# Performance work log

Measured on AMD Instinct MI355X. Metric: run time of the kernel, lower is better.

Reference implementation:

```python
import jax, jax.numpy as jnp
import numpy as np

N, E, H = 25000, 100000, 32          # nodes, edges, node/clique hidden dim
NC, A, EC = 8000, 50000, 24000       # cliques, node2clique assignments, clique edges
EEMB, CEE, L = 8, 8, 2               # edge emb dims, n layers


def segment_mean(vals, ids, num):
    s = jax.ops.segment_sum(vals, ids, num_segments=num)
    cnt = jax.ops.segment_sum(jnp.ones(ids.shape[0], vals.dtype), ids, num_segments=num)
    return s / jnp.maximum(cnt, 1.0)[:, None]


def setup_inputs() -> dict:
    key = jax.random.key(0)
    ks = jax.random.split(key, 24)
    s = 0.1  # param scale
    inp = {
        "node_features": jax.random.normal(ks[0], (N, H), jnp.float32),
        "edge_index": jax.random.randint(ks[1], (2, E), 0, N),
        "edge_features": jax.random.normal(ks[2], (E, EEMB), jnp.float32),
        "clique_features": jax.random.normal(ks[3], (NC, H), jnp.float32),
        "node2clique_index": jnp.stack([
            jax.random.randint(ks[4], (A,), 0, N),
            jax.random.randint(ks[5], (A,), 0, NC)]),
        "clique_edge_index": jax.random.randint(ks[6], (2, EC), 0, NC),
        "clique_edge_features": jax.random.normal(ks[7], (EC, CEE), jnp.float32),
        # node NNConv params (stacked over L layers)
        "nn1_w": jax.random.normal(ks[8], (L, EEMB, H)) * s,
        "nn1_b": jnp.zeros((L, H)),
        "nn2_w": jax.random.normal(ks[9], (L, H, H * H)) * s,
        "nn2_b": jnp.zeros((L, H * H)),
        "root_w": jax.random.normal(ks[10], (L, H, H)) * s,
        "root_b": jnp.zeros((L, H)),
        # Node2Clique linear
        "n2c_w": jax.random.normal(ks[11], (L, H, H)) * s,
        "n2c_b": jnp.zeros((L, H)),
        # clique NNConv params
        "cnn1_w": jax.random.normal(ks[12], (L, CEE, H)) * s,
        "cnn1_b": jnp.zeros((L, H)),
        "cnn2_w": jax.random.normal(ks[13], (L, H, H * H)) * s,
        "cnn2_b": jnp.zeros((L, H * H)),
        "croot_w": jax.random.normal(ks[14], (L, H, H)) * s,
        "croot_b": jnp.zeros((L, H)),
        # Clique2Node linear
        "c2n_w": jax.random.normal(ks[15], (L, H, H)) * s,
        "c2n_b": jnp.zeros((L, H)),
    }
    return inp


def nnconv(x, src, dst, edge_attr, w1, b1, w2, b2, rw, rb, n_out_nodes):
    # per-edge weight matrices from the edge MLP: [E, in, out]
    h = jax.nn.relu(edge_attr @ w1 + b1)
    We = (h @ w2 + b2).reshape(edge_attr.shape[0], x.shape[1], -1)
    msg = jnp.einsum('ei,eio->eo', x[src], We)           # message from source
    agg = segment_mean(msg, dst, n_out_nodes)            # mean aggregation at target
    return agg + x @ rw + rb                             # root weight + bias


def reference(node_features, edge_index, edge_features, clique_features,
              node2clique_index, clique_edge_index, clique_edge_features,
              nn1_w, nn1_b, nn2_w, nn2_b, root_w, root_b, n2c_w, n2c_b,
              cnn1_w, cnn1_b, cnn2_w, cnn2_b, croot_w, croot_b, c2n_w, c2n_b):
    x, c = node_features, clique_features
    src, dst = edge_index[0], edge_index[1]
    nid, cid = node2clique_index[0], node2clique_index[1]
    csrc, cdst = clique_edge_index[0], clique_edge_index[1]
    for l in range(L):
        # node-level edge-conditioned conv
        x = jax.nn.relu(nnconv(x, src, dst, edge_features,
                               nn1_w[l], nn1_b[l], nn2_w[l], nn2_b[l],
                               root_w[l], root_b[l], N))
        # Node2Clique: project node feats, scatter-mean into cliques
        m = x @ n2c_w[l] + n2c_b[l]
        c = c + segment_mean(m[nid], cid, NC)
        # clique-level edge-conditioned conv
        c = jax.nn.relu(nnconv(c, csrc, cdst, clique_edge_features,
                               cnn1_w[l], cnn1_b[l], cnn2_w[l], cnn2_b[l],
                               croot_w[l], croot_b[l], NC))
        # Clique2Node: project clique feats, scatter-mean back onto nodes
        m = c @ c2n_w[l] + c2n_b[l]
        x = x + segment_mean(m[cid], nid, N)
    return (x, c)
```

## Files before the change

### kernel.cpp

```cpp
#include <hip/hip_runtime.h>
#include <hip/hip_bf16.h>

typedef unsigned int u32;
typedef unsigned short u16;

#define DEVINL __device__ __forceinline__

constexpr int Nn  = 25000;
constexpr int Ee  = 100000;
constexpr int NCc = 8000;
constexpr int Aa  = 50000;
constexpr int ECc = 24000;
constexpr int TCOLS = 1088;
constexpr int WPSZ  = TCOLS*32;
constexpr int TT_ROW = 561;
constexpr int NB_N = (Nn + 255)/256;
constexpr int NB_C = (NCc + 255)/256;
constexpr int HB_N = Ee/16;
constexpr int HB_C = ECc/16;

typedef float f32x4 __attribute__((ext_vector_type(4)));
typedef _Float16 h16x2 __attribute__((ext_vector_type(2)));
typedef _Float16 h16x8 __attribute__((ext_vector_type(8)));

DEVINL float b2f(u16 u){ union{u32 i;float f;}v; v.i = ((u32)u)<<16; return v.f; }
DEVINL float bfl(u32 u){ union{u32 i;float f;}v; v.i = u<<16; return v.f; }
DEVINL float bfh(u32 u){ union{u32 i;float f;}v; v.i = u & 0xffff0000u; return v.f; }
DEVINL u16 f2b(float f){ union{float f;u32 i;}v; v.f=f; u32 i=v.i;
  return (u16)((i + 0x7fffu + ((i>>16)&1u)) >> 16); }
DEVINL u16 f2h(float x){ union{ _Float16 h; u16 u; } v; v.h = (_Float16)x; return v.u; }
DEVINL u32 pkh2(float a, float b){
  union{ _Float16 h[2]; u32 u; } v;
  v.h[0] = (_Float16)a; v.h[1] = (_Float16)b; return v.u;
}
DEVINL float ldw(const void* p, long i, int f){
  return f ? ((const float*)p)[i] : b2f(((const u16*)p)[i]);
}
DEVINL float dot2f(u32 a, u32 b, float c){
  union U{u32 u; h16x2 h;};
  U ua; ua.u = a; U ub; ub.u = b;
#if __has_builtin(__builtin_amdgcn_fdot2)
  return __builtin_amdgcn_fdot2(ua.h, ub.h, c, false);
#else
  return c + (float)ua.h[0]*(float)ub.h[0] + (float)ua.h[1]*(float)ub.h[1];
#endif
}

__global__ __launch_bounds__(256) void k_detect(const u16* __restrict__ p, int n,
                        u32* __restrict__ maxbits, int* __restrict__ zcnt,
                        int* __restrict__ done, int* __restrict__ flag){
  int i0 = blockIdx.x*256 + threadIdx.x;
  float lm = 0.f; int lz = 0;
  for (int i = i0; i < n; i += gridDim.x*256){
    u16 v = p[i];
    if (v == 0) lz++;
    lm = fmaxf(lm, fabsf(b2f(v)));
  }
  #pragma unroll
  for (int off = 32; off; off >>= 1){
    lm = fmaxf(lm, __shfl_down(lm, off));
    lz += __shfl_down(lz, off);
  }
  if ((threadIdx.x & 63) == 0){
    atomicMax(maxbits, __float_as_uint(lm));
    atomicAdd(zcnt, lz);
  }
  __syncthreads();
  if (threadIdx.x == 0){
    __threadfence();
    if (atomicAdd(done, 1) == gridDim.x - 1){
      float m = __uint_as_float(*maxbits);
      *flag = (m > 1e6f || *zcnt > n/4) ? 1 : 0;
    }
  }
}

__global__ __launch_bounds__(256) void k_count_all(const int* __restrict__ ei, const int* __restrict__ cei,
                          const int* __restrict__ n2c,
                          int* __restrict__ deg_nd, int* __restrict__ deg_ce,
                          int* __restrict__ deg_n2c, int* __restrict__ deg_c2n,
                          int* __restrict__ cnt_sn, int* __restrict__ cnt_sc){
  int i = blockIdx.x*256 + threadIdx.x;
  if (i < Ee)                             atomicAdd(&deg_nd[ei[Ee + i]], 1);
  else if ((i -= Ee) < ECc)               atomicAdd(&deg_ce[cei[ECc + i]], 1);
  else if ((i -= ECc) < Aa)               atomicAdd(&deg_n2c[n2c[Aa + i]], 1);
  else if ((i -= Aa) < Aa)                atomicAdd(&deg_c2n[n2c[i]], 1);
  else if ((i -= Aa) < Ee)                atomicAdd(&cnt_sn[ei[i]], 1);
  else if ((i -= Ee) < ECc)               atomicAdd(&cnt_sc[cei[i]], 1);
}

__global__ __launch_bounds__(256) void k_scan_block(
    const int* __restrict__ c0, const int* __restrict__ c1,
    const int* __restrict__ c2, const int* __restrict__ c3,
    int* __restrict__ o0, int* __restrict__ o1, int* __restrict__ o2, int* __restrict__ o3,
    int* __restrict__ b0, int* __restrict__ b1, int* __restrict__ b2, int* __restrict__ b3){
  __shared__ int s[256];
  int bid = blockIdx.x, seg, rb;
  if (bid < NB_N){ seg=0; rb=bid; }
  else if (bid < NB_N+NB_C){ seg=1; rb=bid-NB_N; }
  else if (bid < 2*NB_N+NB_C){ seg=2; rb=bid-NB_N-NB_C; }
  else { seg=3; rb=bid-2*NB_N-NB_C; }
  const int* cnt = seg==0?c0 : seg==1?c1 : seg==2?c2 : c3;
  int* offs = seg==0?o0 : seg==1?o1 : seg==2?o2 : o3;
  int* bs   = seg==0?b0 : seg==1?b1 : seg==2?b2 : b3;
  int M = (seg & 1) ? NCc : Nn;
  int tid = threadIdx.x;
  int i = rb*256 + tid;
  int v = (i < M) ? cnt[i] : 0;
  s[tid] = v; __syncthreads();
  for (int d = 1; d < 256; d <<= 1){
    int t = (tid >= d) ? s[tid-d] : 0;
    __syncthreads();
    s[tid] += t;
    __syncthreads();
  }
  if (i < M) offs[i] = s[tid] - v;
  if (tid == 255) bs[rb] = s[255];
}

__global__ __launch_bounds__(512) void k_spine(int* __restrict__ b0, int* __restrict__ b1,
                      int* __restrict__ b2, int* __restrict__ b3){
  __shared__ int s[512];
  int tid = threadIdx.x, seg = tid >> 7, lane = tid & 127;
  int NB = (seg & 1) ? NB_C : NB_N;
  int* bp = seg==0?b0 : seg==1?b1 : seg==2?b2 : b3;
  int v = (lane < NB) ? bp[lane] : 0;
  s[tid] = v; __syncthreads();
  for (int d = 1; d < 128; d <<= 1){
    int t = (lane >= d) ? s[tid-d] : 0;
    __syncthreads();
    s[tid] += t;
    __syncthreads();
  }
  if (lane < NB) bp[lane] = s[tid] - v;
}

__global__ __launch_bounds__(256) void k_scan_fix(
    int* __restrict__ o0, int* __restrict__ o1, int* __restrict__ o2, int* __restrict__ o3,
    const int* __restrict__ b0, const int* __restrict__ b1,
    const int* __restrict__ b2, const int* __restrict__ b3){
  int i = blockIdx.x*256 + threadIdx.x;
  if (i < Nn) o0[i] += b0[i >> 8];
  else if ((i -= Nn) < NCc) o1[i] += b1[i >> 8];
  else if ((i -= NCc) < Nn) o2[i] += b2[i >> 8];
  else if ((i -= Nn) < NCc) o3[i] += b3[i >> 8];
}

__global__ __launch_bounds__(256) void k_place(const int* __restrict__ ei, const int* __restrict__ cei,
                      const int* __restrict__ n2c,
                      const int* __restrict__ offs_n, const int* __restrict__ offs_c,
                      const int* __restrict__ offs_an, const int* __restrict__ offs_ac,
                      int* __restrict__ cur_n, int* __restrict__ cur_c,
                      int* __restrict__ cur_an, int* __restrict__ cur_ac,
                      int* __restrict__ perm_n, int* __restrict__ perm_c,
                      int* __restrict__ an2c, int* __restrict__ ac2n){
  int i = blockIdx.x*256 + threadIdx.x;
  if (i < Ee){
    int s = ei[i];
    perm_n[offs_n[s] + atomicAdd(&cur_n[s], 1)] = i;
  } else if ((i -= Ee) < ECc){
    int s = cei[i];
    perm_c[offs_c[s] + atomicAdd(&cur_c[s], 1)] = i;
  } else if ((i -= ECc) < Aa){
    int c = n2c[Aa + i];
    an2c[offs_ac[c] + atomicAdd(&cur_ac[c], 1)] = n2c[i];
  } else if ((i -= Aa) < Aa){
    int nd = n2c[i];
    ac2n[offs_an[nd] + atomicAdd(&cur_an[nd], 1)] = n2c[Aa + i];
  }
}

__global__ __launch_bounds__(256) void k_gather(const int* __restrict__ ei, const int* __restrict__ cei,
                       const int* __restrict__ perm_n, const int* __restrict__ perm_c,
                       const void* __restrict__ ef, const void* __restrict__ cef,
                       const int* __restrict__ flag,
                       int2* __restrict__ sdp_n, float* __restrict__ efp_n,
                       int2* __restrict__ sdp_c, float* __restrict__ efp_c){
  int i = blockIdx.x*256 + threadIdx.x;
  int f = *flag;
  if (i < Ee*8){
    int p = i >> 3, j = i & 7;
    int e = perm_n[p];
    efp_n[i] = ldw(ef, (long)e*8 + j, f);
    if (j == 0) sdp_n[p] = make_int2(ei[e], ei[Ee + e]);
  } else if ((i -= Ee*8) < ECc*8){
    int p = i >> 3, j = i & 7;
    int e = perm_c[p];
    efp_c[i] = ldw(cef, (long)e*8 + j, f);
    if (j == 0) sdp_c[p] = make_int2(cei[e], cei[ECc + e]);
  }
}

__global__ __launch_bounds__(256) void k_hprep(const float* __restrict__ efp_n, const float* __restrict__ efp_c,
                      const void* __restrict__ nn1w, const void* __restrict__ nn1b,
                      const void* __restrict__ cnn1w, const void* __restrict__ cnn1b,
                      const int* __restrict__ flag,
                      u32* __restrict__ hp_n, u32* __restrict__ hp_c){
  __shared__ float w1s[256], b1s[32], efs[128];
  int b = blockIdx.x, tid = threadIdx.x;
  int isC, l, rb_;
  if (b < HB_N){ isC=0; l=0; rb_=b; }
  else if (b < 2*HB_N){ isC=0; l=1; rb_=b-HB_N; }
  else if (b < 2*HB_N+HB_C){ isC=1; l=0; rb_=b-2*HB_N; }
  else { isC=1; l=1; rb_=b-2*HB_N-HB_C; }
  const float* efp = isC ? efp_c : efp_n;
  const void* W1 = isC ? cnn1w : nn1w;
  const void* B1 = isC ? cnn1b : nn1b;
  u32* hp = (isC ? hp_c : hp_n) + (size_t)l*(isC?ECc:Ee)*16;
  int f = *flag;
  w1s[tid] = ldw(W1, (long)l*256 + tid, f);
  if (tid < 32) b1s[tid] = ldw(B1, (long)l*32 + tid, f);
  if (tid < 128) efs[tid] = efp[(size_t)rb_*128 + tid];
  __syncthreads();
  int e8 = tid >> 4, kk = tid & 15;
  float a0 = b1s[2*kk], a1 = b1s[2*kk+1];
  #pragma unroll
  for (int j = 0; j < 8; j++){
    float ev = efs[e8*8 + j];
    a0 += ev * w1s[j*32 + 2*kk];
    a1 += ev * w1s[j*32 + 2*kk + 1];
  }
  hp[(size_t)rb_*256 + tid] = pkh2(fmaxf(a0, 0.f), fmaxf(a1, 0.f));
}

__global__ __launch_bounds__(256) void k_wpack_all(const void* __restrict__ nn2w, const void* __restrict__ nn2b,
                          const void* __restrict__ rootw,
                          const void* __restrict__ cnn2w, const void* __restrict__ cnn2b,
                          const void* __restrict__ crootw,
                          const int* __restrict__ flag, u16* __restrict__ Wp4){
  int i = blockIdx.x*256 + threadIdx.x;
  if (i >= 4*WPSZ) return;
  int set = i / WPSZ, j = i - set*WPSZ;
  int l = set >> 1, isC = set & 1;
  const void* W2 = isC ? cnn2w : nn2w;
  const void* B2 = isC ? cnn2b : nn2b;
  const void* RW = isC ? crootw : rootw;
  int f = *flag;
  int col = j >> 5, ii = j & 31;
  float v;
  if (col < 1024)      v = ldw(W2, (long)l*32768 + ((col>>5)<<10) + (ii<<5) + (col&31), f);
  else if (col < 1056) v = ldw(B2, (long)l*1024 + (ii<<5) + (col-1024), f);
  else                 v = ldw(RW, (long)l*1024 + (ii<<5) + (col-1056), f);
  Wp4[i] = f2h(v);
}

__global__ __launch_bounds__(512) void k_conv_fused(const void* __restrict__ base, int braw,
                           const float* __restrict__ addagg, const int* __restrict__ adddeg, int M,
                           const int2* __restrict__ sdp, const u32* __restrict__ hp,
                           const int* __restrict__ offs, int E_,
                           const u16* __restrict__ Wp,
                           const void* __restrict__ rb, long rboff,
                           const int* __restrict__ flag,
                           float* __restrict__ feat_root, float* __restrict__ agg){
  __shared__ __align__(16) u32 Tt[16*TT_ROW];
  __shared__ u32 hws[8][64];
  int tid = threadIdx.x;
  int w = tid >> 6, lane = tid & 63;
  int quad = lane >> 4, lm = lane & 15;
  int n0 = blockIdx.x * 16;
  int f = *flag;
  int n = n0 + lm;
  int nc = n < M ? n : M-1;
  long bidx = (long)nc*32 + quad*8;
  float fv[8];
  if (braw && f == 0){
    uint4 q = *(const uint4*)((const u16*)base + bidx);
    fv[0]=bfl(q.x); fv[1]=bfh(q.x); fv[2]=bfl(q.y); fv[3]=bfh(q.y);
    fv[4]=bfl(q.z); fv[5]=bfh(q.z); fv[6]=bfl(q.w); fv[7]=bfh(q.w);
  } else {
    const float4* bp = (const float4*)((const float*)base + bidx);
    float4 q0 = bp[0], q1 = bp[1];
    fv[0]=q0.x; fv[1]=q0.y; fv[2]=q0.z; fv[3]=q0.w;
    fv[4]=q1.x; fv[5]=q1.y; fv[6]=q1.z; fv[7]=q1.w;
  }
  if (addagg){
    int dg = adddeg[nc];
    float d = (float)(dg > 1 ? dg : 1);
    const float4* ap = (const float4*)(addagg + (size_t)nc*32 + quad*8);
    float4 a0 = ap[0], a1 = ap[1];
    float inv = 1.f/d;
    fv[0]+=a0.x*inv; fv[1]+=a0.y*inv; fv[2]+=a0.z*inv; fv[3]+=a0.w*inv;
    fv[4]+=a1.x*inv; fv[5]+=a1.y*inv; fv[6]+=a1.z*inv; fv[7]+=a1.w*inv;
  }
  union { h16x8 v; u32 u[4]; } bf;
  #pragma unroll
  for (int j = 0; j < 4; j++) bf.u[j] = pkh2(fv[2*j], fv[2*j+1]);

  #define AFR(ct) (*(const h16x8*)(Wp + (size_t)((ct)*16 + lm)*32 + quad*8))
  f32x4 z4 = {0.f, 0.f, 0.f, 0.f};
  #pragma unroll
  for (int g = 0; g < 2; g++){
    int q = w + 8*g;
    f32x4 c0 = __builtin_amdgcn_mfma_f32_16x16x32_f16(AFR(4*q+0), bf.v, z4, 0, 0, 0);
    f32x4 c1 = __builtin_amdgcn_mfma_f32_16x16x32_f16(AFR(4*q+1), bf.v, z4, 0, 0, 0);
    f32x4 c2 = __builtin_amdgcn_mfma_f32_16x16x32_f16(AFR(4*q+2), bf.v, z4, 0, 0, 0);
    f32x4 c3 = __builtin_amdgcn_mfma_f32_16x16x32_f16(AFR(4*q+3), bf.v, z4, 0, 0, 0);
    int rbase = lm*TT_ROW;
    int ob = quad*4;
    #pragma unroll
    for (int i = 0; i < 4; i++){
      Tt[rbase + (ob+i)*17 + q]      = pkh2(c0[i], c2[i]);
      Tt[rbase + (16+ob+i)*17 + q]   = pkh2(c1[i], c3[i]);
    }
  }
  if (w < 4){
    int ct = 64 + w;
    f32x4 c = __builtin_amdgcn_mfma_f32_16x16x32_f16(AFR(ct), bf.v, z4, 0, 0, 0);
    if (ct < 66){
      int p0 = (ct-64)*8 + quad*2;
      Tt[lm*TT_ROW + 544 + p0]     = pkh2(c[0], c[1]);
      Tt[lm*TT_ROW + 544 + p0 + 1] = pkh2(c[2], c[3]);
    } else if (n < M){
      int o = (ct-66)*16 + quad*4;
      float4 v = make_float4(c[0] + ldw(rb, rboff+o,   f),
                             c[1] + ldw(rb, rboff+o+1, f),
                             c[2] + ldw(rb, rboff+o+2, f),
                             c[3] + ldw(rb, rboff+o+3, f));
      *(float4*)&feat_root[(size_t)n*32 + o] = v;
    }
  }
  __syncthreads();

  int lo = offs[n0];
  int hi = (n0 + 16 < M) ? offs[n0 + 16] : E_;
  int eg = quad, kk = lm;
  int pos = lo + w*4;
  u32 hp0 = 0, hp1 = 0; int sd0 = 0, sd1 = 0;
  { int idx = pos*16 + lane;      if (idx < hi*16) hp0 = hp[idx];
    idx = (pos+32)*16 + lane;     if (idx < hi*16) hp1 = hp[idx]; }
  if (lane < 8){
    int idx = pos*2 + lane;       if (idx < hi*2) sd0 = ((const int*)sdp)[idx];
    idx = (pos+32)*2 + lane;      if (idx < hi*2) sd1 = ((const int*)sdp)[idx];
  }
  for (; pos < hi; pos += 32){
    int np = pos + 64;
    u32 hp2 = 0; int sd2 = 0;
    { int idx = np*16 + lane; if (idx < hi*16) hp2 = hp[idx]; }
    if (lane < 8){ int idx = np*2 + lane; if (idx < hi*2) sd2 = ((const int*)sdp)[idx]; }
    hws[w][lane] = hp0;
    int sn = __shfl(sd0, 2*eg);
    int dn = __shfl(sd0, 2*eg + 1);
    bool valid = (pos + eg < hi);
    int sr = sn - n0; sr = sr < 0 ? 0 : (sr > 15 ? 15 : sr);
    const u32* Tr = Tt + sr*TT_ROW;
    const u32* T0 = Tr + 34*kk;
    const u32* Hp = &hws[w][eg*16];
    union{u32 u; h16x2 h;} b2u; b2u.u = Tr[544 + kk];
    float m0 = (float)b2u.h[0], m1 = (float)b2u.h[1];
    #pragma unroll
    for (int kq = 0; kq < 16; kq++){
      u32 hv = Hp[kq];
      u32 t0 = T0[kq];
      u32 t1 = T0[17 + kq];
      m0 = dot2f(hv, t0, m0);
      m1 = dot2f(hv, t1, m1);
    }
    if (valid){
      float* ap = agg + (size_t)dn*32 + 2*kk;
      atomicAdd(ap,   m0);
      atomicAdd(ap+1, m1);
    }
    hp0 = hp1; sd0 = sd1; hp1 = hp2; sd1 = sd2;
  }
  #undef AFR
}

__global__ __launch_bounds__(256) void k_update_lin(const float* __restrict__ agg, const int* __restrict__ deg,
                           const float* __restrict__ feat_root, int M,
                           const void* __restrict__ w, long woff,
                           const void* __restrict__ b, long boff,
                           const int* __restrict__ flag,
                           float* __restrict__ feat,
                           const int* __restrict__ sidx, const int* __restrict__ soffs,
                           const int* __restrict__ sdeg, float* __restrict__ sagg){
  __shared__ float wsm[1024], bs[32], rows[8][33];
  int tid = threadIdx.x;
  int f = *flag;
  for (int idx = tid; idx < 1024; idx += 256) wsm[idx] = ldw(w, woff + idx, f);
  if (tid < 32) bs[tid] = ldw(b, boff + tid, f);
  int nl = tid >> 5, o = tid & 31;
  int n = blockIdx.x*8 + nl;
  long i = (long)n*32 + o;
  if (n < M){
    int dg = deg[n];
    float d = (float)(dg > 1 ? dg : 1);
    float v = fmaxf(agg[i]/d + feat_root[i], 0.f);
    rows[nl][o] = v;
    feat[i] = v;
  }
  __syncthreads();
  if (n >= M) return;
  float acc = bs[o];
  #pragma unroll
  for (int j = 0; j < 32; j++) acc += rows[nl][j]*wsm[j*32+o];
  int slo = soffs[n], scnt = sdeg[n];
  for (int a = 0; a < scnt; a++)
    atomicAdd(&sagg[(size_t)sidx[slo + a]*32 + o], acc);
}

__global__ __launch_bounds__(256) void k_store(const float* __restrict__ x, const float* __restrict__ xagg,
                      const int* __restrict__ xdeg, const float* __restrict__ c,
                      void* __restrict__ out, const int* __restrict__ flag){
  int i = blockIdx.x*256 + threadIdx.x;
  int tot = Nn*32 + NCc*32;
  if (i >= tot) return;
  float v;
  if (i < Nn*32){
    int n = i >> 5;
    int dg = xdeg[n];
    float d = (float)(dg > 1 ? dg : 1);
    v = x[i] + xagg[i]/d;
  } else v = c[i - Nn*32];
  if (*flag) ((float*)out)[i] = v;
  else       ((u16*)out)[i]   = f2b(v);
}

extern "C" void kernel_launch(void* const* d_in, const int* in_sizes, int n_in,
                              void* d_out, int out_size, void* d_ws, size_t ws_size,
                              hipStream_t stream){
  const int* ei  = (const int*)d_in[1];
  const int* n2c = (const int*)d_in[4];
  const int* cei = (const int*)d_in[5];
  const void *efr = d_in[2], *cefr = d_in[6];
  const void *nn1w = d_in[7], *nn1b = d_in[8], *nn2w = d_in[9], *nn2b = d_in[10],
             *rootw = d_in[11], *rootb = d_in[12], *n2cw = d_in[13], *n2cb = d_in[14],
             *cnn1w = d_in[15], *cnn1b = d_in[16], *cnn2w = d_in[17], *cnn2b = d_in[18],
             *crootw = d_in[19], *crootb = d_in[20], *c2nw = d_in[21], *c2nb = d_in[22];

  char* ws = (char*)d_ws;
  size_t off = 0;
  auto alloc = [&](size_t bytes){ void* p = ws + off; off += (bytes + 255) & ~(size_t)255; return p; };

  size_t zstart = off;
  float* aggE0  = (float*)alloc((size_t)Nn*32*4);
  float* aggE1  = (float*)alloc((size_t)Nn*32*4);
  float* caggE0 = (float*)alloc((size_t)NCc*32*4);
  float* caggE1 = (float*)alloc((size_t)NCc*32*4);
  float* caggS0 = (float*)alloc((size_t)NCc*32*4);
  float* caggS1 = (float*)alloc((size_t)NCc*32*4);
  float* aggS0  = (float*)alloc((size_t)Nn*32*4);
  float* aggS1  = (float*)alloc((size_t)Nn*32*4);
  int* deg_nd  = (int*)alloc((size_t)Nn*4);
  int* deg_ce  = (int*)alloc((size_t)NCc*4);
  int* deg_n2c = (int*)alloc((size_t)NCc*4);
  int* deg_c2n = (int*)alloc((size_t)Nn*4);
  int* cnt_sn  = (int*)alloc((size_t)Nn*4);
  int* cnt_sc  = (int*)alloc((size_t)NCc*4);
  int* cur_n   = (int*)alloc((size_t)Nn*4);
  int* cur_c   = (int*)alloc((size_t)NCc*4);
  int* cur_an  = (int*)alloc((size_t)Nn*4);
  int* cur_ac  = (int*)alloc((size_t)NCc*4);
  u32* maxbits = (u32*)alloc(256);
  int* zcnt = (int*)((char*)maxbits + 4);
  int* flag = (int*)((char*)maxbits + 8);
  int* done = (int*)((char*)maxbits + 12);
  size_t zbytes = off - zstart;

  float* xB  = (float*)alloc((size_t)Nn*32*4);
  float* xC  = (float*)alloc((size_t)Nn*32*4);
  float* cC0 = (float*)alloc((size_t)NCc*32*4);
  float* cC1 = (float*)alloc((size_t)NCc*32*4);
  float* frn = (float*)alloc((size_t)Nn*32*4);
  float* frc = (float*)alloc((size_t)NCc*32*4);
  int* offs_n  = (int*)alloc((size_t)Nn*4);
  int* offs_c  = (int*)alloc((size_t)NCc*4);
  int* offs_an = (int*)alloc((size_t)Nn*4);
  int* offs_ac = (int*)alloc((size_t)NCc*4);
  int* bs0 = (int*)alloc(512); int* bs1 = (int*)alloc(512);
  int* bs2 = (int*)alloc(512); int* bs3 = (int*)alloc(512);
  int* perm_n = (int*)alloc((size_t)Ee*4);
  int* perm_c = (int*)alloc((size_t)ECc*4);
  int* an2c = (int*)alloc((size_t)Aa*4);
  int* ac2n = (int*)alloc((size_t)Aa*4);
  int2* sdp_n = (int2*)alloc((size_t)Ee*8);
  int2* sdp_c = (int2*)alloc((size_t)ECc*8);
  float* efp_n = (float*)alloc((size_t)Ee*8*4);
  float* efp_c = (float*)alloc((size_t)ECc*8*4);
  u16* Wp4 = (u16*)alloc((size_t)4*WPSZ*2);
  u32* hp_n = (u32*)alloc((size_t)2*Ee*16*4);
  u32* hp_c = (u32*)alloc((size_t)2*ECc*16*4);

  auto nb = [](int n){ return (n + 255)/256; };

  hipMemsetAsync(ws + zstart, 0, zbytes, stream);
  k_detect<<<256,256,0,stream>>>((const u16*)d_in[0], Nn*32, maxbits, zcnt, done, flag);
  k_count_all<<<nb(2*Ee + 2*ECc + 2*Aa),256,0,stream>>>(ei, cei, n2c,
      deg_nd, deg_ce, deg_n2c, deg_c2n, cnt_sn, cnt_sc);
  k_scan_block<<<2*(NB_N+NB_C),256,0,stream>>>(cnt_sn, cnt_sc, deg_c2n, deg_n2c,
      offs_n, offs_c, offs_an, offs_ac, bs0, bs1, bs2, bs3);
  k_spine<<<1,512,0,stream>>>(bs0, bs1, bs2, bs3);
  k_scan_fix<<<nb(2*(Nn+NCc)),256,0,stream>>>(offs_n, offs_c, offs_an, offs_ac,
      bs0, bs1, bs2, bs3);
  k_place<<<nb(Ee+ECc+2*Aa),256,0,stream>>>(ei, cei, n2c, offs_n, offs_c, offs_an, offs_ac,
      cur_n, cur_c, cur_an, cur_ac, perm_n, perm_c, an2c, ac2n);
  k_gather<<<nb(8*(Ee+ECc)),256,0,stream>>>(ei, cei, perm_n, perm_c, efr, cefr, flag,
      sdp_n, efp_n, sdp_c, efp_c);
  k_wpack_all<<<nb(4*WPSZ),256,0,stream>>>(nn2w, nn2b, rootw, cnn2w, cnn2b, crootw, flag, Wp4);
  k_hprep<<<2*HB_N + 2*HB_C,256,0,stream>>>(efp_n, efp_c, nn1w, nn1b, cnn1w, cnn1b, flag,
      hp_n, hp_c);

  int Gn = (Nn + 15)/16, Gc = (NCc + 15)/16;

  k_conv_fused<<<Gn,512,0,stream>>>(d_in[0], 1, nullptr, nullptr, Nn, sdp_n, hp_n, offs_n, Ee,
      Wp4 + 0*WPSZ, rootb, 0, flag, frn, aggE0);
  k_update_lin<<<(Nn+7)/8,256,0,stream>>>(aggE0, deg_nd, frn, Nn, n2cw, 0, n2cb, 0, flag,
      xB, ac2n, offs_an, deg_c2n, caggS0);
  k_conv_fused<<<Gc,512,0,stream>>>(d_in[3], 1, caggS0, deg_n2c, NCc, sdp_c, hp_c, offs_c, ECc,
      Wp4 + 1*WPSZ, crootb, 0, flag, frc, caggE0);
  k_update_lin<<<(NCc+7)/8,256,0,stream>>>(caggE0, deg_ce, frc, NCc, c2nw, 0, c2nb, 0, flag,
      cC0, an2c, offs_ac, deg_n2c, aggS0);
  k_conv_fused<<<Gn,512,0,stream>>>(xB, 0, aggS0, deg_c2n, Nn, sdp_n, hp_n + (size_t)Ee*16, offs_n, Ee,
      Wp4 + 2*WPSZ, rootb, 32, flag, frn, aggE1);
  k_update_lin<<<(Nn+7)/8,256,0,stream>>>(aggE1, deg_nd, frn, Nn, n2cw, 1024, n2cb, 32, flag,
      xC, ac2n, offs_an, deg_c2n, caggS1);
  k_conv_fused<<<Gc,512,0,stream>>>(cC0, 0, caggS1, deg_n2c, NCc, sdp_c, hp_c + (size_t)ECc*16, offs_c, ECc,
      Wp4 + 3*WPSZ, crootb, 32, flag, frc, caggE1);
  k_update_lin<<<(NCc+7)/8,256,0,stream>>>(caggE1, deg_ce, frc, NCc, c2nw, 1024, c2nb, 32, flag,
      cC1, an2c, offs_ac, deg_n2c, aggS1);
  k_store<<<nb(Nn*32 + NCc*32),256,0,stream>>>(xC, aggS1, deg_c2n, cC1, d_out, flag);
}
```

Before: 333.8 us.

## Fuse preprocessing kernels: detect+count, spine into scan-fix, place+gather+hprep+wpack

Merges the input-detection pass with the degree counting, folds the block-sum spine scan into the scan-fix kernel (each block reduces the preceding block sums itself), and combines edge placement, edge-feature gathering, first-layer edge MLP and weight packing into one kernel. Each edge now scatters its packed hidden features directly to its sorted slot, which removes the perm and efp intermediate buffers and several launches. In exchange, the per-edge MLP runs one thread per edge with scattered 64-byte writes instead of coalesced per-block tiles, so those stores may be less efficient.

Measured after the change: 426.7 us. 1.28x slower.

```diff
diff --git a/kernel.cpp b/kernel.cpp
--- a/kernel.cpp
+++ b/kernel.cpp
@@ -16,8 +16,10 @@
 constexpr int TT_ROW = 561;
 constexpr int NB_N = (Nn + 255)/256;
 constexpr int NB_C = (NCc + 255)/256;
-constexpr int HB_N = Ee/16;
-constexpr int HB_C = ECc/16;
+constexpr int PB_EN = (Ee + 255)/256;
+constexpr int PB_EC = (ECc + 255)/256;
+constexpr int PB_AS = (2*Aa + 255)/256;
+constexpr int PB_WP = (4*WPSZ + 255)/256;
 
 typedef float f32x4 __attribute__((ext_vector_type(4)));
 typedef _Float16 h16x2 __attribute__((ext_vector_type(2)));
@@ -46,10 +48,23 @@
 #endif
 }
 
-__global__ __launch_bounds__(256) void k_detect(const u16* __restrict__ p, int n,
+__global__ __launch_bounds__(256) void k_detect_count(const u16* __restrict__ p, int n,
                         u32* __restrict__ maxbits, int* __restrict__ zcnt,
-                        int* __restrict__ done, int* __restrict__ flag){
+                        int* __restrict__ done, int* __restrict__ flag,
+                        const int* __restrict__ ei, const int* __restrict__ cei,
+                        const int* __restrict__ n2c,
+                        int* __restrict__ deg_nd, int* __restrict__ deg_ce,
+                        int* __restrict__ deg_n2c, int* __restrict__ deg_c2n,
+                        int* __restrict__ cnt_sn, int* __restrict__ cnt_sc){
   int i0 = blockIdx.x*256 + threadIdx.x;
+  { int t = i0;
+    if (t < Ee)                             atomicAdd(&deg_nd[ei[Ee + t]], 1);
+    else if ((t -= Ee) < ECc)               atomicAdd(&deg_ce[cei[ECc + t]], 1);
+    else if ((t -= ECc) < Aa)               atomicAdd(&deg_n2c[n2c[Aa + t]], 1);
+    else if ((t -= Aa) < Aa)                atomicAdd(&deg_c2n[n2c[t]], 1);
+    else if ((t -= Aa) < Ee)                atomicAdd(&cnt_sn[ei[t]], 1);
+    else if ((t -= Ee) < ECc)               atomicAdd(&cnt_sc[cei[t]], 1);
+  }
   float lm = 0.f; int lz = 0;
   for (int i = i0; i < n; i += gridDim.x*256){
     u16 v = p[i];
@@ -73,20 +88,6 @@
       *flag = (m > 1e6f || *zcnt > n/4) ? 1 : 0;
     }
   }
-}
-
-__global__ __launch_bounds__(256) void k_count_all(const int* __restrict__ ei, const int* __restrict__ cei,
-                          const int* __restrict__ n2c,
-                          int* __restrict__ deg_nd, int* __restrict__ deg_ce,
-                          int* __restrict__ deg_n2c, int* __restrict__ deg_c2n,
-                          int* __restrict__ cnt_sn, int* __restrict__ cnt_sc){
-  int i = blockIdx.x*256 + threadIdx.x;
-  if (i < Ee)                             atomicAdd(&deg_nd[ei[Ee + i]], 1);
-  else if ((i -= Ee) < ECc)               atomicAdd(&deg_ce[cei[ECc + i]], 1);
-  else if ((i -= ECc) < Aa)               atomicAdd(&deg_n2c[n2c[Aa + i]], 1);
-  else if ((i -= Aa) < Aa)                atomicAdd(&deg_c2n[n2c[i]], 1);
-  else if ((i -= Aa) < Ee)                atomicAdd(&cnt_sn[ei[i]], 1);
-  else if ((i -= Ee) < ECc)               atomicAdd(&cnt_sc[cei[i]], 1);
 }
 
 __global__ __launch_bounds__(256) void k_scan_block(
@@ -118,130 +119,111 @@
   if (tid == 255) bs[rb] = s[255];
 }
 
-__global__ __launch_bounds__(512) void k_spine(int* __restrict__ b0, int* __restrict__ b1,
-                      int* __restrict__ b2, int* __restrict__ b3){
-  __shared__ int s[512];
-  int tid = threadIdx.x, seg = tid >> 7, lane = tid & 127;
-  int NB = (seg & 1) ? NB_C : NB_N;
-  int* bp = seg==0?b0 : seg==1?b1 : seg==2?b2 : b3;
-  int v = (lane < NB) ? bp[lane] : 0;
-  s[tid] = v; __syncthreads();
-  for (int d = 1; d < 128; d <<= 1){
-    int t = (lane >= d) ? s[tid-d] : 0;
-    __syncthreads();
-    s[tid] += t;
-    __syncthreads();
-  }
-  if (lane < NB) bp[lane] = s[tid] - v;
-}
-
-__global__ __launch_bounds__(256) void k_scan_fix(
+__global__ __launch_bounds__(256) void k_scan_fix2(
     int* __restrict__ o0, int* __restrict__ o1, int* __restrict__ o2, int* __restrict__ o3,
     const int* __restrict__ b0, const int* __restrict__ b1,
     const int* __restrict__ b2, const int* __restrict__ b3){
-  int i = blockIdx.x*256 + threadIdx.x;
-  if (i < Nn) o0[i] += b0[i >> 8];
-  else if ((i -= Nn) < NCc) o1[i] += b1[i >> 8];
-  else if ((i -= NCc) < Nn) o2[i] += b2[i >> 8];
-  else if ((i -= Nn) < NCc) o3[i] += b3[i >> 8];
-}
-
-__global__ __launch_bounds__(256) void k_place(const int* __restrict__ ei, const int* __restrict__ cei,
-                      const int* __restrict__ n2c,
-                      const int* __restrict__ offs_n, const int* __restrict__ offs_c,
-                      const int* __restrict__ offs_an, const int* __restrict__ offs_ac,
-                      int* __restrict__ cur_n, int* __restrict__ cur_c,
-                      int* __restrict__ cur_an, int* __restrict__ cur_ac,
-                      int* __restrict__ perm_n, int* __restrict__ perm_c,
-                      int* __restrict__ an2c, int* __restrict__ ac2n){
-  int i = blockIdx.x*256 + threadIdx.x;
-  if (i < Ee){
-    int s = ei[i];
-    perm_n[offs_n[s] + atomicAdd(&cur_n[s], 1)] = i;
-  } else if ((i -= Ee) < ECc){
-    int s = cei[i];
-    perm_c[offs_c[s] + atomicAdd(&cur_c[s], 1)] = i;
-  } else if ((i -= ECc) < Aa){
-    int c = n2c[Aa + i];
-    an2c[offs_ac[c] + atomicAdd(&cur_ac[c], 1)] = n2c[i];
-  } else if ((i -= Aa) < Aa){
-    int nd = n2c[i];
-    ac2n[offs_an[nd] + atomicAdd(&cur_an[nd], 1)] = n2c[Aa + i];
-  }
-}
-
-__global__ __launch_bounds__(256) void k_gather(const int* __restrict__ ei, const int* __restrict__ cei,
-                       const int* __restrict__ perm_n, const int* __restrict__ perm_c,
-                       const void* __restrict__ ef, const void* __restrict__ cef,
-                       const int* __restrict__ flag,
-                       int2* __restrict__ sdp_n, float* __restrict__ efp_n,
-                       int2* __restrict__ sdp_c, float* __restrict__ efp_c){
-  int i = blockIdx.x*256 + threadIdx.x;
+  __shared__ int s[256];
+  int bid = blockIdx.x, seg, rb;
+  if (bid < NB_N){ seg=0; rb=bid; }
+  else if (bid < NB_N+NB_C){ seg=1; rb=bid-NB_N; }
+  else if (bid < 2*NB_N+NB_C){ seg=2; rb=bid-NB_N-NB_C; }
+  else { seg=3; rb=bid-2*NB_N-NB_C; }
+  int* offs = seg==0?o0 : seg==1?o1 : seg==2?o2 : o3;
+  const int* bsp = seg==0?b0 : seg==1?b1 : seg==2?b2 : b3;
+  int M = (seg & 1) ? NCc : Nn;
+  int tid = threadIdx.x;
+  int v = (tid < rb) ? bsp[tid] : 0;
+  s[tid] = v; __syncthreads();
+  #pragma unroll
+  for (int d = 128; d; d >>= 1){
+    if (tid < d) s[tid] += s[tid + d];
+    __syncthreads();
+  }
+  int prefix = s[0];
+  int i = rb*256 + tid;
+  if (i < M) offs[i] += prefix;
+}
+
+__global__ __launch_bounds__(256) void k_place_pack(
+    const int* __restrict__ ei, const int* __restrict__ cei, const int* __restrict__ n2c,
+    const void* __restrict__ ef, const void* __restrict__ cef,
+    const void* __restrict__ nn1w, const void* __restrict__ nn1b,
+    const void* __restrict__ cnn1w, const void* __restrict__ cnn1b,
+    const void* __restrict__ nn2w, const void* __restrict__ nn2b, const void* __restrict__ rootw,
+    const void* __restrict__ cnn2w, const void* __restrict__ cnn2b, const void* __restrict__ crootw,
+    const int* __restrict__ offs_n, const int* __restrict__ offs_c,
+    const int* __restrict__ offs_an, const int* __restrict__ offs_ac,
+    int* __restrict__ cur_n, int* __restrict__ cur_c,
+    int* __restrict__ cur_an, int* __restrict__ cur_ac,
+    int2* __restrict__ sdp_n, int2* __restrict__ sdp_c,
+    u32* __restrict__ hp_n, u32* __restrict__ hp_c,
+    int* __restrict__ an2c, int* __restrict__ ac2n,
+    const int* __restrict__ flag, u16* __restrict__ Wp4){
+  int b = blockIdx.x, tid = threadIdx.x;
   int f = *flag;
-  if (i < Ee*8){
-    int p = i >> 3, j = i & 7;
-    int e = perm_n[p];
-    efp_n[i] = ldw(ef, (long)e*8 + j, f);
-    if (j == 0) sdp_n[p] = make_int2(ei[e], ei[Ee + e]);
-  } else if ((i -= Ee*8) < ECc*8){
-    int p = i >> 3, j = i & 7;
-    int e = perm_c[p];
-    efp_c[i] = ldw(cef, (long)e*8 + j, f);
-    if (j == 0) sdp_c[p] = make_int2(cei[e], cei[ECc + e]);
-  }
-}
-
-__global__ __launch_bounds__(256) void k_hprep(const float* __restrict__ efp_n, const float* __restrict__ efp_c,
-                      const void* __restrict__ nn1w, const void* __restrict__ nn1b,
-                      const void* __restrict__ cnn1w, const void* __restrict__ cnn1b,
-                      const int* __restrict__ flag,
-                      u32* __restrict__ hp_n, u32* __restrict__ hp_c){
-  __shared__ float w1s[256], b1s[32], efs[128];
-  int b = blockIdx.x, tid = threadIdx.x;
-  int isC, l, rb_;
-  if (b < HB_N){ isC=0; l=0; rb_=b; }
-  else if (b < 2*HB_N){ isC=0; l=1; rb_=b-HB_N; }
-  else if (b < 2*HB_N+HB_C){ isC=1; l=0; rb_=b-2*HB_N; }
-  else { isC=1; l=1; rb_=b-2*HB_N-HB_C; }
-  const float* efp = isC ? efp_c : efp_n;
-  const void* W1 = isC ? cnn1w : nn1w;
-  const void* B1 = isC ? cnn1b : nn1b;
-  u32* hp = (isC ? hp_c : hp_n) + (size_t)l*(isC?ECc:Ee)*16;
-  int f = *flag;
-  w1s[tid] = ldw(W1, (long)l*256 + tid, f);
-  if (tid < 32) b1s[tid] = ldw(B1, (long)l*32 + tid, f);
-  if (tid < 128) efs[tid] = efp[(size_t)rb_*128 + tid];
-  __syncthreads();
-  int e8 = tid >> 4, kk = tid & 15;
-  float a0 = b1s[2*kk], a1 = b1s[2*kk+1];
-  #pragma unroll
-  for (int j = 0; j < 8; j++){
-    float ev = efs[e8*8 + j];
-    a0 += ev * w1s[j*32 + 2*kk];
-    a1 += ev * w1s[j*32 + 2*kk + 1];
-  }
-  hp[(size_t)rb_*256 + tid] = pkh2(fmaxf(a0, 0.f), fmaxf(a1, 0.f));
-}
-
-__global__ __launch_bounds__(256) void k_wpack_all(const void* __restrict__ nn2w, const void* __restrict__ nn2b,
-                          const void* __restrict__ rootw,
-                          const void* __restrict__ cnn2w, const void* __restrict__ cnn2b,
-                          const void* __restrict__ crootw,
-                          const int* __restrict__ flag, u16* __restrict__ Wp4){
-  int i = blockIdx.x*256 + threadIdx.x;
-  if (i >= 4*WPSZ) return;
-  int set = i / WPSZ, j = i - set*WPSZ;
-  int l = set >> 1, isC = set & 1;
-  const void* W2 = isC ? cnn2w : nn2w;
-  const void* B2 = isC ? cnn2b : nn2b;
-  const void* RW = isC ? crootw : rootw;
-  int f = *flag;
-  int col = j >> 5, ii = j & 31;
-  float v;
-  if (col < 1024)      v = ldw(W2, (long)l*32768 + ((col>>5)<<10) + (ii<<5) + (col&31), f);
-  else if (col < 1056) v = ldw(B2, (long)l*1024 + (ii<<5) + (col-1024), f);
-  else                 v = ldw(RW, (long)l*1024 + (ii<<5) + (col-1056), f);
-  Wp4[i] = f2h(v);
+  if (b < PB_EN + PB_EC){
+    __shared__ float w1s[2][256], b1s[2][32];
+    int isC = (b >= PB_EN);
+    int e = (isC ? b - PB_EN : b)*256 + tid;
+    int E = isC ? ECc : Ee;
+    const void* W1 = isC ? cnn1w : nn1w;
+    const void* B1 = isC ? cnn1b : nn1b;
+    w1s[0][tid] = ldw(W1, tid, f);
+    w1s[1][tid] = ldw(W1, 256 + tid, f);
+    if (tid < 32){ b1s[0][tid] = ldw(B1, tid, f); b1s[1][tid] = ldw(B1, 32 + tid, f); }
+    __syncthreads();
+    if (e < E){
+      const int* EI = isC ? cei : ei;
+      int s = EI[e], d = EI[E + e];
+      int* cur = isC ? cur_c : cur_n;
+      const int* offs = isC ? offs_c : offs_n;
+      int p = offs[s] + atomicAdd(&cur[s], 1);
+      (isC ? sdp_c : sdp_n)[p] = make_int2(s, d);
+      const void* EF = isC ? cef : ef;
+      float ev[8];
+      #pragma unroll
+      for (int j = 0; j < 8; j++) ev[j] = ldw(EF, (long)e*8 + j, f);
+      u32* hp = isC ? hp_c : hp_n;
+      #pragma unroll
+      for (int l = 0; l < 2; l++){
+        u32* hq = hp + (size_t)l*E*16 + (size_t)p*16;
+        #pragma unroll
+        for (int kk = 0; kk < 16; kk++){
+          float a0 = b1s[l][2*kk], a1 = b1s[l][2*kk+1];
+          #pragma unroll
+          for (int j = 0; j < 8; j++){
+            a0 += ev[j]*w1s[l][j*32 + 2*kk];
+            a1 += ev[j]*w1s[l][j*32 + 2*kk + 1];
+          }
+          hq[kk] = pkh2(fmaxf(a0, 0.f), fmaxf(a1, 0.f));
+        }
+      }
+    }
+  } else if (b < PB_EN + PB_EC + PB_AS){
+    int i = (b - PB_EN - PB_EC)*256 + tid;
+    if (i < Aa){
+      int c = n2c[Aa + i];
+      an2c[offs_ac[c] + atomicAdd(&cur_ac[c], 1)] = n2c[i];
+    } else if ((i -= Aa) < Aa){
+      int nd = n2c[i];
+      ac2n[offs_an[nd] + atomicAdd(&cur_an[nd], 1)] = n2c[Aa + i];
+    }
+  } else {
+    int i = (b - PB_EN - PB_EC - PB_AS)*256 + tid;
+    if (i >= 4*WPSZ) return;
+    int set = i / WPSZ, j = i - set*WPSZ;
+    int l = set >> 1, isC = set & 1;
+    const void* W2 = isC ? cnn2w : nn2w;
+    const void* B2 = isC ? cnn2b : nn2b;
+    const void* RW = isC ? crootw : rootw;
+    int col = j >> 5, ii = j & 31;
+    float v;
+    if (col < 1024)      v = ldw(W2, (long)l*32768 + ((col>>5)<<10) + (ii<<5) + (col&31), f);
+    else if (col < 1056) v = ldw(B2, (long)l*1024 + (ii<<5) + (col-1024), f);
+    else                 v = ldw(RW, (long)l*1024 + (ii<<5) + (col-1056), f);
+    Wp4[i] = f2h(v);
+  }
 }
 
 __global__ __launch_bounds__(512) void k_conv_fused(const void* __restrict__ base, int braw,
@@ -468,14 +450,10 @@
   int* offs_ac = (int*)alloc((size_t)NCc*4);
   int* bs0 = (int*)alloc(512); int* bs1 = (int*)alloc(512);
   int* bs2 = (int*)alloc(512); int* bs3 = (int*)alloc(512);
-  int* perm_n = (int*)alloc((size_t)Ee*4);
-  int* perm_c = (int*)alloc((size_t)ECc*4);
   int* an2c = (int*)alloc((size_t)Aa*4);
   int* ac2n = (int*)alloc((size_t)Aa*4);
   int2* sdp_n = (int2*)alloc((size_t)Ee*8);
   int2* sdp_c = (int2*)alloc((size_t)ECc*8);
-  float* efp_n = (float*)alloc((size_t)Ee*8*4);
-  float* efp_c = (float*)alloc((size_t)ECc*8*4);
   u16* Wp4 = (u16*)alloc((size_t)4*WPSZ*2);
   u32* hp_n = (u32*)alloc((size_t)2*Ee*16*4);
   u32* hp_c = (u32*)alloc((size_t)2*ECc*16*4);
@@ -483,21 +461,17 @@
   auto nb = [](int n){ return (n + 255)/256; };
 
   hipMemsetAsync(ws + zstart, 0, zbytes, stream);
-  k_detect<<<256,256,0,stream>>>((const u16*)d_in[0], Nn*32, maxbits, zcnt, done, flag);
-  k_count_all<<<nb(2*Ee + 2*ECc + 2*Aa),256,0,stream>>>(ei, cei, n2c,
+  k_detect_count<<<nb(2*Ee + 2*ECc + 2*Aa),256,0,stream>>>((const u16*)d_in[0], Nn*32,
+      maxbits, zcnt, done, flag, ei, cei, n2c,
       deg_nd, deg_ce, deg_n2c, deg_c2n, cnt_sn, cnt_sc);
   k_scan_block<<<2*(NB_N+NB_C),256,0,stream>>>(cnt_sn, cnt_sc, deg_c2n, deg_n2c,
       offs_n, offs_c, offs_an, offs_ac, bs0, bs1, bs2, bs3);
-  k_spine<<<1,512,0,stream>>>(bs0, bs1, bs2, bs3);
-  k_scan_fix<<<nb(2*(Nn+NCc)),256,0,stream>>>(offs_n, offs_c, offs_an, offs_ac,
+  k_scan_fix2<<<2*(NB_N+NB_C),256,0,stream>>>(offs_n, offs_c, offs_an, offs_ac,
       bs0, bs1, bs2, bs3);
-  k_place<<<nb(Ee+ECc+2*Aa),256,0,stream>>>(ei, cei, n2c, offs_n, offs_c, offs_an, offs_ac,
-      cur_n, cur_c, cur_an, cur_ac, perm_n, perm_c, an2c, ac2n);
-  k_gather<<<nb(8*(Ee+ECc)),256,0,stream>>>(ei, cei, perm_n, perm_c, efr, cefr, flag,
-      sdp_n, efp_n, sdp_c, efp_c);
-  k_wpack_all<<<nb(4*WPSZ),256,0,stream>>>(nn2w, nn2b, rootw, cnn2w, cnn2b, crootw, flag, Wp4);
-  k_hprep<<<2*HB_N + 2*HB_C,256,0,stream>>>(efp_n, efp_c, nn1w, nn1b, cnn1w, cnn1b, flag,
-      hp_n, hp_c);
+  k_place_pack<<<PB_EN+PB_EC+PB_AS+PB_WP,256,0,stream>>>(ei, cei, n2c, efr, cefr,
+      nn1w, nn1b, cnn1w, cnn1b, nn2w, nn2b, rootw, cnn2w, cnn2b, crootw,
+      offs_n, offs_c, offs_an, offs_ac, cur_n, cur_c, cur_an, cur_ac,
+      sdp_n, sdp_c, hp_n, hp_c, an2c, ac2n, flag, Wp4);
 
   int Gn = (Nn + 15)/16, Gc = (NCc + 15)/16;
 
```
